# Kernel tuning notes

Measured on AMD Instinct MI355X. Metric: run time of the kernel, lower is better.

The kernel has to match this reference:

```python
import jax, jax.numpy as jnp
import numpy as np

N, D, K, P = 4096, 256, 16, 3
MAXDEG = K + 1          # self loop guarantees deg >= 1, randint caps deg <= K+1
TAU, LAM, BETA, MARGIN = 0.8, 0.5, 1.0, 0.1
EPS_PD = 1e-6           # F.pairwise_distance eps (added to the difference)


def _make_adj(k):
    nbr = jax.random.randint(k, (N, K), 0, N)
    m = jnp.zeros((N, N), jnp.float32)
    m = m.at[jnp.arange(N)[:, None], nbr].set(1.0)
    m = m.at[jnp.arange(N), jnp.arange(N)].set(1.0)
    return m / m.sum(1, keepdims=True)  # row-normalized metapath adjacency


def setup_inputs():
    key = jax.random.key(0)
    ks = jax.random.split(key, 12)
    g = 1.414 * (2.0 / (D + D)) ** 0.5  # xavier_normal gain=1.414
    return {
        "h": jax.random.normal(ks[0], (N, D), jnp.float32),
        "mps": jnp.stack([_make_adj(ks[1 + i]) for i in range(P)]),
        "W_gcn": jax.random.normal(ks[4], (P, D, D), jnp.float32) * g,
        "b_gcn": jnp.zeros((P, D), jnp.float32),
        "prelu_a": jnp.full((P,), 0.25, jnp.float32),
        "att_fc_W": jax.random.normal(ks[5], (D, D), jnp.float32) * g,
        "att_fc_b": jnp.zeros((D,), jnp.float32),
        "att_vec": jax.random.normal(ks[6], (D,), jnp.float32) * g,
        "proj_W1": jax.random.normal(ks[7], (D, D), jnp.float32) * g,
        "proj_b1": jnp.zeros((D,), jnp.float32),
        "proj_W2": jax.random.normal(ks[8], (D, D), jnp.float32) * g,
        "proj_b2": jnp.zeros((D,), jnp.float32),
    }


def _gcn(h, adj, W, b, a):
    out = adj @ (h @ W.T) + b          # spmm(adj, fc(h)) + bias
    return jnp.where(out > 0, out, a * out)  # PReLU


def _node_loss(emb, adj):
    # vectorized form of the per-node nonzero/pairwise_distance loop
    mask = adj > 0                      # [N, N]
    deg = mask.sum(1)                   # [N], >= 1 via self loops
    # stable argsort: neighbors first (ascending index), matching torch.nonzero order
    pos_idx = jnp.argsort(~mask, axis=1)[:, :MAXDEG]
    neg_idx = jnp.argsort(mask, axis=1)[:, :MAXDEG]   # first deg non-neighbors
    anc = emb[:, None, :]               # anchor expanded over pairs
    dp = jnp.sum((anc - emb[pos_idx] + EPS_PD) ** 2, -1)  # [N, MAXDEG]
    dn = jnp.sum((anc - emb[neg_idx] + EPS_PD) ** 2, -1)
    valid = jnp.arange(MAXDEG)[None, :] < deg[:, None]
    per = jnp.maximum(dp - dn + MARGIN, 0.0) * valid
    return jnp.sum(per.sum(1) / deg.astype(emb.dtype))  # per-node mean, summed


def _proj(z, W1, b1, W2, b2):
    return jax.nn.elu(z @ W1.T + b1) @ W2.T + b2


def _contrast(z1, z2, pos, W1, b1, W2, b2):
    p1 = _proj(z1, W1, b1, W2, b2)
    p2 = _proj(z2, W1, b1, W2, b2)
    n1 = jnp.linalg.norm(p1, axis=-1, keepdims=True)
    n2 = jnp.linalg.norm(p2, axis=-1, keepdims=True)
    sim = jnp.exp((p1 @ p2.T) / (n1 * n2.T) / TAU)     # [N, N]
    m12 = sim / (sim.sum(1, keepdims=True) + 1e-8)
    m21 = sim.T / (sim.T.sum(1, keepdims=True) + 1e-8)
    l12 = -jnp.log((m12 * pos).sum(-1)).mean()
    l21 = -jnp.log((m21 * pos).sum(-1)).mean()
    return LAM * l12 + (1.0 - LAM) * l21


def reference(h, mps, W_gcn, b_gcn, prelu_a, att_fc_W, att_fc_b, att_vec,
              proj_W1, proj_b1, proj_W2, proj_b2):
    embeds = [_gcn(h, mps[i], W_gcn[i], b_gcn[i], prelu_a[i]) for i in range(P)]
    node_loss = sum(_node_loss(embeds[i], mps[i]) for i in range(P))
    # faithful to original control flow: i==0 inner loop overwrites self.loss,
    # so only the (0, P-1) pair survives from i==0
    closs = _contrast(embeds[0], embeds[P - 1], mps[0], proj_W1, proj_b1, proj_W2, proj_b2)
    for i in range(1, P - 1):
        for j in range(i + 1, P):
            closs = closs + _contrast(embeds[i], embeds[j], mps[i], proj_W1, proj_b1, proj_W2, proj_b2)
    # semantic attention over metapaths
    sp = jnp.stack([jnp.tanh(e @ att_fc_W.T + att_fc_b).mean(0) for e in embeds])  # [P, D]
    beta = jax.nn.softmax(sp @ att_vec)                                            # [P]
    z_mp = jnp.einsum('p,pnd->nd', beta, jnp.stack(embeds))
    return z_mp, node_loss + BETA * closs
```

## Files before the change

kernel.cpp:

```cpp
#include <hip/hip_runtime.h>
#include <hip/hip_bf16.h>

constexpr int N = 4096;
constexpr int D = 256;
constexpr int P = 3;
constexpr int MAXDEG = 17;
constexpr float TAU = 0.8f;
constexpr float MARGIN = 0.1f;
constexpr float EPS_PD = 1e-6f;

constexpr int LDP = 40;

constexpr int OFF_H    = 0;
constexpr int OFF_WG   = 1048576;
constexpr int OFF_ATTW = 1245184;
constexpr int OFF_W1   = 1310720;
constexpr int OFF_W2   = 1376256;
constexpr int OFF_BG   = 1441792;
constexpr int OFF_ATTB = 1442560;
constexpr int OFF_AV   = 1442816;
constexpr int OFF_PA   = 1443072;
constexpr int OFF_B1   = 1443328;
constexpr int OFF_B2   = 1443584;
constexpr int CONV_TOTAL = 1443840;

typedef __attribute__((ext_vector_type(8))) short bfrag8;
typedef __attribute__((ext_vector_type(4))) float facc4;

__device__ inline facc4 mfma16(bfrag8 a, bfrag8 b, facc4 c) {
    return __builtin_amdgcn_mfma_f32_16x16x32_bf16(a, b, c, 0, 0, 0);
}
__device__ inline float b2f(__hip_bfloat16 v) { return __bfloat162float(v); }
__device__ inline float bfbits2f(unsigned short u) {
    return __uint_as_float(((unsigned int)u) << 16);
}
__device__ inline unsigned short f2bfbits(float v) {
    __hip_bfloat16 t = __float2bfloat16(v);
    return *(unsigned short*)&t;
}
__device__ inline int get_bf(const int* __restrict__ counter) { return counter[0] > 100; }

__device__ inline float load_in(const void* p, size_t i, int bf) {
    return bf ? __bfloat162float(((const __hip_bfloat16*)p)[i])
              : ((const float*)p)[i];
}

__device__ __forceinline__ void gl_lds16(const __hip_bfloat16* g, __hip_bfloat16* l) {
    __builtin_amdgcn_global_load_lds(
        (const __attribute__((address_space(1))) unsigned int*)g,
        (__attribute__((address_space(3))) unsigned int*)l, 16, 0, 0);
}

__global__ void detect_dtype(const unsigned int* __restrict__ w, int nwords,
                             int* __restrict__ counter,
                             float* __restrict__ zbuf, int nz) {
    int t0 = blockIdx.x * blockDim.x + threadIdx.x;
    if (t0 < nz) zbuf[t0] = 0.f;
    int stride = gridDim.x * blockDim.x;
    int c = 0;
    for (int i = t0; i < nwords; i += stride) {
        unsigned int x = w[i];
        if ((x & 0xFFFF0000u) == 0u && x != 0u) c++;
    }
    for (int s = 32; s > 0; s >>= 1) c += __shfl_down(c, s);
    if ((threadIdx.x & 63) == 0 && c > 0) atomicMax(counter, 1 << 20);
}

__global__ void stage2(const void* __restrict__ h, const void* __restrict__ wg,
                       const void* __restrict__ mps,
                       const void* attw, const void* w1, const void* w2,
                       const void* bg, const void* attb, const void* av,
                       const void* pa, const void* b1, const void* b2,
                       const int* __restrict__ counter,
                       __hip_bfloat16* __restrict__ conv,
                       __hip_bfloat16* __restrict__ xbuf,
                       int* __restrict__ nbr_idx, float* __restrict__ nbr_val,
                       int* __restrict__ neg_idx, int* __restrict__ deg) {
    __shared__ __align__(16) __hip_bfloat16 As[64 * LDP];
    __shared__ __align__(16) __hip_bfloat16 Bs[3][64 * LDP];
    int bid = blockIdx.x;
    int bf = get_bf(counter);
    if (bid < 256) {
        int bm = (bid & 63) * 64, bn = (bid >> 6) * 64;
        int tid = threadIdx.x, wave = tid >> 6, lane = tid & 63;
        int quad = lane >> 4, l15 = lane & 15;
        int wr = (wave & 1) * 32, wc = (wave >> 1) * 32;
        facc4 acc[3][2][2] = {};
        int sr = tid >> 2, kq = (tid & 3) * 8;
        for (int k0 = 0; k0 < D; k0 += 32) {
            if (bf) {
                *(bfrag8*)&As[sr * LDP + kq] =
                    *(const bfrag8*)((const unsigned short*)h + (size_t)(bm + sr) * D + k0 + kq);
                #pragma unroll
                for (int z = 0; z < 3; z++)
                    *(bfrag8*)&Bs[z][sr * LDP + kq] =
                        *(const bfrag8*)((const unsigned short*)wg +
                                         (size_t)z * D * D + (size_t)(bn + sr) * D + k0 + kq);
            } else {
                const float* hp = (const float*)h + (size_t)(bm + sr) * D + k0 + kq;
                float4 a0 = *(const float4*)hp, a1 = *(const float4*)(hp + 4);
                bfrag8 t;
                t[0] = f2bfbits(a0.x); t[1] = f2bfbits(a0.y);
                t[2] = f2bfbits(a0.z); t[3] = f2bfbits(a0.w);
                t[4] = f2bfbits(a1.x); t[5] = f2bfbits(a1.y);
                t[6] = f2bfbits(a1.z); t[7] = f2bfbits(a1.w);
                *(bfrag8*)&As[sr * LDP + kq] = t;
                #pragma unroll
                for (int z = 0; z < 3; z++) {
                    const float* wp = (const float*)wg +
                        (size_t)z * D * D + (size_t)(bn + sr) * D + k0 + kq;
                    float4 b0 = *(const float4*)wp, b1v = *(const float4*)(wp + 4);
                    bfrag8 u;
                    u[0] = f2bfbits(b0.x);  u[1] = f2bfbits(b0.y);
                    u[2] = f2bfbits(b0.z);  u[3] = f2bfbits(b0.w);
                    u[4] = f2bfbits(b1v.x); u[5] = f2bfbits(b1v.y);
                    u[6] = f2bfbits(b1v.z); u[7] = f2bfbits(b1v.w);
                    *(bfrag8*)&Bs[z][sr * LDP + kq] = u;
                }
            }
            __syncthreads();
            bfrag8 af[2];
            #pragma unroll
            for (int mi = 0; mi < 2; mi++)
                af[mi] = *(const bfrag8*)&As[(wr + mi * 16 + l15) * LDP + quad * 8];
            #pragma unroll
            for (int z = 0; z < 3; z++) {
                bfrag8 bfr[2];
                #pragma unroll
                for (int ni = 0; ni < 2; ni++)
                    bfr[ni] = *(const bfrag8*)&Bs[z][(wc + ni * 16 + l15) * LDP + quad * 8];
                #pragma unroll
                for (int mi = 0; mi < 2; mi++)
                    #pragma unroll
                    for (int ni = 0; ni < 2; ni++)
                        acc[z][mi][ni] = mfma16(af[mi], bfr[ni], acc[z][mi][ni]);
            }
            __syncthreads();
        }
        #pragma unroll
        for (int z = 0; z < 3; z++)
            #pragma unroll
            for (int mi = 0; mi < 2; mi++)
                #pragma unroll
                for (int ni = 0; ni < 2; ni++) {
                    int col = bn + wc + ni * 16 + l15;
                    #pragma unroll
                    for (int r = 0; r < 4; r++) {
                        int row = bm + wr + mi * 16 + quad * 4 + r;
                        xbuf[(size_t)z * N * D + (size_t)row * D + col] =
                            __float2bfloat16(acc[z][mi][ni][r]);
                    }
                }
    } else if (bid < 256 + P * N) {
        int row = bid - 256;
        int t = threadIdx.x;
        int* cnt = (int*)As;
        int* sidx = ((int*)As) + 1;
        float* sval = (float*)(((int*)As) + 33);
        if (t == 0) *cnt = 0;
        __syncthreads();
        int e0 = t * 16;
        if (bf) {
            const uint4* base = (const uint4*)((const __hip_bfloat16*)mps + (size_t)row * N + e0);
            #pragma unroll
            for (int v = 0; v < 2; v++) {
                uint4 w = base[v];
                unsigned int ws[4] = {w.x, w.y, w.z, w.w};
                #pragma unroll
                for (int j = 0; j < 4; j++) {
                    unsigned short lo = (unsigned short)(ws[j] & 0xFFFFu);
                    unsigned short hi = (unsigned short)(ws[j] >> 16);
                    if (lo) { int k = atomicAdd(cnt, 1); if (k < 32) { sidx[k] = e0 + v * 8 + j * 2;     sval[k] = bfbits2f(lo); } }
                    if (hi) { int k = atomicAdd(cnt, 1); if (k < 32) { sidx[k] = e0 + v * 8 + j * 2 + 1; sval[k] = bfbits2f(hi); } }
                }
            }
        } else {
            const float4* base = (const float4*)((const float*)mps + (size_t)row * N + e0);
            #pragma unroll
            for (int v = 0; v < 4; v++) {
                float4 w = base[v];
                float ws[4] = {w.x, w.y, w.z, w.w};
                #pragma unroll
                for (int j = 0; j < 4; j++)
                    if (ws[j] > 0.f) { int k = atomicAdd(cnt, 1); if (k < 32) { sidx[k] = e0 + v * 4 + j; sval[k] = ws[j]; } }
            }
        }
        __syncthreads();
        if (t < 64) {
            int dg = *cnt; if (dg > MAXDEG) dg = MAXDEG;
            int myidx = 0; float myval = 0.f; int rank = 0;
            if (t < dg) {
                myidx = sidx[t]; myval = sval[t];
                for (int j = 0; j < dg; j++) rank += (sidx[j] < myidx) ? 1 : 0;
            }
            if (t < dg) { sidx[rank] = myidx; sval[rank] = myval; }
            if (t < MAXDEG) {
                nbr_idx[(size_t)row * MAXDEG + t] = (t < dg) ? sidx[t] : 0;
                nbr_val[(size_t)row * MAXDEG + t] = (t < dg) ? sval[t] : 0.f;
            }
            if (t == 0) deg[row] = dg;
            int c = t;
            bool cand = (c < dg + MAXDEG);
            bool isnbr = false;
            if (cand) for (int j = 0; j < dg; j++) isnbr |= (sidx[j] == c);
            bool nonnbr = cand && !isnbr;
            unsigned long long m = __ballot(nonnbr);
            int nrank = __popcll(m & ((c < 64) ? ((1ull << c) - 1ull) : ~0ull));
            if (nonnbr && nrank < MAXDEG) neg_idx[(size_t)row * MAXDEG + nrank] = c;
        }
    } else {
        int cb = bid - (256 + P * N);
        const void* srcs[9] = {attw, w1, w2, bg, attb, av, pa, b1, b2};
        const int offs[9] = {OFF_ATTW, OFF_W1, OFF_W2, OFF_BG, OFF_ATTB,
                             OFF_AV, OFF_PA, OFF_B1, OFF_B2};
        const int lens[9] = {65536, 65536, 65536, 768, 256, 256, 3, 256, 256};
        int stride = 64 * 256;
        int t0 = cb * 256 + threadIdx.x;
        #pragma unroll
        for (int s = 0; s < 9; s++) {
            for (int i = t0; i < lens[s]; i += stride)
                conv[offs[s] + i] = __float2bfloat16(load_in(srcs[s], i, bf));
        }
    }
}

__global__ void spmm_prelu(const __hip_bfloat16* __restrict__ Xbase,
                           const int* __restrict__ nbr_idx, const float* __restrict__ nbr_val,
                           const int* __restrict__ deg, const __hip_bfloat16* __restrict__ conv,
                           __hip_bfloat16* __restrict__ embBase) {
    int z = blockIdx.z;
    int wave = threadIdx.x >> 6, lane = threadIdx.x & 63;
    int n = blockIdx.x * 4 + wave;
    const __hip_bfloat16* X = Xbase + (size_t)z * N * D;
    int dg = deg[z * N + n];
    int idxv = 0; float valv = 0.f;
    if (lane < MAXDEG) {
        idxv = nbr_idx[((size_t)z * N + n) * MAXDEG + lane];
        valv = nbr_val[((size_t)z * N + n) * MAXDEG + lane];
    }
    float acc[4] = {0.f, 0.f, 0.f, 0.f};
    int k = 0;
    for (; k + 3 < dg; k += 4) {
        int j0 = __shfl(idxv, k), j1 = __shfl(idxv, k + 1);
        int j2 = __shfl(idxv, k + 2), j3 = __shfl(idxv, k + 3);
        float v0 = __shfl(valv, k), v1 = __shfl(valv, k + 1);
        float v2 = __shfl(valv, k + 2), v3 = __shfl(valv, k + 3);
        ushort4 x0 = *(const ushort4*)&X[(size_t)j0 * D + lane * 4];
        ushort4 x1 = *(const ushort4*)&X[(size_t)j1 * D + lane * 4];
        ushort4 x2 = *(const ushort4*)&X[(size_t)j2 * D + lane * 4];
        ushort4 x3 = *(const ushort4*)&X[(size_t)j3 * D + lane * 4];
        acc[0] += v0 * bfbits2f(x0.x) + v1 * bfbits2f(x1.x) + v2 * bfbits2f(x2.x) + v3 * bfbits2f(x3.x);
        acc[1] += v0 * bfbits2f(x0.y) + v1 * bfbits2f(x1.y) + v2 * bfbits2f(x2.y) + v3 * bfbits2f(x3.y);
        acc[2] += v0 * bfbits2f(x0.z) + v1 * bfbits2f(x1.z) + v2 * bfbits2f(x2.z) + v3 * bfbits2f(x3.z);
        acc[3] += v0 * bfbits2f(x0.w) + v1 * bfbits2f(x1.w) + v2 * bfbits2f(x2.w) + v3 * bfbits2f(x3.w);
    }
    for (; k < dg; k++) {
        int j0 = __shfl(idxv, k); float v0 = __shfl(valv, k);
        ushort4 x0 = *(const ushort4*)&X[(size_t)j0 * D + lane * 4];
        acc[0] += v0 * bfbits2f(x0.x); acc[1] += v0 * bfbits2f(x0.y);
        acc[2] += v0 * bfbits2f(x0.z); acc[3] += v0 * bfbits2f(x0.w);
    }
    ushort4 bb = *(const ushort4*)&conv[OFF_BG + z * D + lane * 4];
    float a = b2f(conv[OFF_PA + z]);
    ushort4 o;
    float v0 = acc[0] + bfbits2f(bb.x); o.x = f2bfbits(v0 > 0.f ? v0 : a * v0);
    float v1 = acc[1] + bfbits2f(bb.y); o.y = f2bfbits(v1 > 0.f ? v1 : a * v1);
    float v2 = acc[2] + bfbits2f(bb.z); o.z = f2bfbits(v2 > 0.f ? v2 : a * v2);
    float v3 = acc[3] + bfbits2f(bb.w); o.w = f2bfbits(v3 > 0.f ? v3 : a * v3);
    *(ushort4*)&embBase[(size_t)z * N * D + (size_t)n * D + lane * 4] = o;
}

__global__ void gemm_dual_nl(const __hip_bfloat16* __restrict__ embBase,
                             const __hip_bfloat16* __restrict__ conv,
                             __hip_bfloat16* __restrict__ xbuf,
                             float* __restrict__ spacc,
                             const int* __restrict__ nbr_idx,
                             const int* __restrict__ neg_idx,
                             const int* __restrict__ deg,
                             float* __restrict__ nlpart) {
    __shared__ __align__(16) __hip_bfloat16 As[64 * LDP];
    __shared__ __align__(16) __hip_bfloat16 Bsa[64 * LDP];
    __shared__ __align__(16) __hip_bfloat16 Bsw[64 * LDP];
    int z = blockIdx.z;
    if (blockIdx.y < 4) {
        const __hip_bfloat16* A = embBase + (size_t)z * N * D;
        const __hip_bfloat16* Ba = conv + OFF_ATTW;
        const __hip_bfloat16* Bw = conv + OFF_W1;
        int bm = blockIdx.x * 64, bn = blockIdx.y * 64;
        int tid = threadIdx.x, wave = tid >> 6, lane = tid & 63;
        int quad = lane >> 4, l15 = lane & 15;
        int wr = (wave & 1) * 32, wc = (wave >> 1) * 32;
        facc4 accA[2][2] = {};
        facc4 accW[2][2] = {};
        int sr = tid >> 2, kq = (tid & 3) * 8;
        for (int k0 = 0; k0 < D; k0 += 32) {
            *(bfrag8*)&As[sr * LDP + kq]  = *(const bfrag8*)&A[(size_t)(bm + sr) * D + k0 + kq];
            *(bfrag8*)&Bsa[sr * LDP + kq] = *(const bfrag8*)&Ba[(size_t)(bn + sr) * D + k0 + kq];
            *(bfrag8*)&Bsw[sr * LDP + kq] = *(const bfrag8*)&Bw[(size_t)(bn + sr) * D + k0 + kq];
            __syncthreads();
            bfrag8 af[2], ba[2], bw[2];
            #pragma unroll
            for (int mi = 0; mi < 2; mi++)
                af[mi] = *(const bfrag8*)&As[(wr + mi * 16 + l15) * LDP + quad * 8];
            #pragma unroll
            for (int ni = 0; ni < 2; ni++) {
                ba[ni] = *(const bfrag8*)&Bsa[(wc + ni * 16 + l15) * LDP + quad * 8];
                bw[ni] = *(const bfrag8*)&Bsw[(wc + ni * 16 + l15) * LDP + quad * 8];
            }
            #pragma unroll
            for (int mi = 0; mi < 2; mi++)
                #pragma unroll
                for (int ni = 0; ni < 2; ni++) {
                    accA[mi][ni] = mfma16(af[mi], ba[ni], accA[mi][ni]);
                    accW[mi][ni] = mfma16(af[mi], bw[ni], accW[mi][ni]);
                }
            __syncthreads();
        }
        float cs[2] = {0.f, 0.f};
        #pragma unroll
        for (int mi = 0; mi < 2; mi++) {
            #pragma unroll
            for (int ni = 0; ni < 2; ni++) {
                int col = bn + wc + ni * 16 + l15;
                float battb = b2f(conv[OFF_ATTB + col]);
                float bb1   = b2f(conv[OFF_B1 + col]);
                #pragma unroll
                for (int r = 0; r < 4; r++) {
                    int row = bm + wr + mi * 16 + quad * 4 + r;
                    cs[ni] += tanhf(accA[mi][ni][r] + battb);
                    float v = accW[mi][ni][r] + bb1;
                    v = v > 0.f ? v : expm1f(v);
                    xbuf[(size_t)z * N * D + (size_t)row * D + col] = __float2bfloat16(v);
                }
            }
        }
        #pragma unroll
        for (int ni = 0; ni < 2; ni++) {
            float v = cs[ni];
            v += __shfl_xor(v, 16); v += __shfl_xor(v, 32);
            if (quad == 0) {
                int col = bn + wc + ni * 16 + l15;
                atomicAdd(&spacc[(size_t)z * D + col], v);
            }
        }
    } else {
        int wave = threadIdx.x >> 6, lane = threadIdx.x & 63;
        int nb = blockIdx.x * 16 + (blockIdx.y - 4);
        int n = nb * 4 + wave;
        const __hip_bfloat16* emb = embBase + (size_t)z * N * D;
        int dg = deg[z * N + n];
        int ipv = 0, igv = 0;
        if (lane < MAXDEG) {
            ipv = nbr_idx[((size_t)z * N + n) * MAXDEG + lane];
            igv = neg_idx[((size_t)z * N + n) * MAXDEG + lane];
        }
        ushort4 ar = *(const ushort4*)&emb[(size_t)n * D + lane * 4];
        float a[4] = {bfbits2f(ar.x), bfbits2f(ar.y), bfbits2f(ar.z), bfbits2f(ar.w)};
        float s = 0.f;
        int k = 0;
        for (; k + 1 < dg; k += 2) {
            int jp0 = __shfl(ipv, k), jn0 = __shfl(igv, k);
            int jp1 = __shfl(ipv, k + 1), jn1 = __shfl(igv, k + 1);
            ushort4 pr0 = *(const ushort4*)&emb[(size_t)jp0 * D + lane * 4];
            ushort4 nr0 = *(const ushort4*)&emb[(size_t)jn0 * D + lane * 4];
            ushort4 pr1 = *(const ushort4*)&emb[(size_t)jp1 * D + lane * 4];
            ushort4 nr1 = *(const ushort4*)&emb[(size_t)jn1 * D + lane * 4];
            float dp0, dn0, dp1, dn1;
            {
                float x0 = a[0] - bfbits2f(pr0.x) + EPS_PD, y0 = a[0] - bfbits2f(nr0.x) + EPS_PD;
                float x1 = a[1] - bfbits2f(pr0.y) + EPS_PD, y1 = a[1] - bfbits2f(nr0.y) + EPS_PD;
                float x2 = a[2] - bfbits2f(pr0.z) + EPS_PD, y2 = a[2] - bfbits2f(nr0.z) + EPS_PD;
                float x3 = a[3] - bfbits2f(pr0.w) + EPS_PD, y3 = a[3] - bfbits2f(nr0.w) + EPS_PD;
                dp0 = x0 * x0 + x1 * x1 + x2 * x2 + x3 * x3;
                dn0 = y0 * y0 + y1 * y1 + y2 * y2 + y3 * y3;
            }
            {
                float x0 = a[0] - bfbits2f(pr1.x) + EPS_PD, y0 = a[0] - bfbits2f(nr1.x) + EPS_PD;
                float x1 = a[1] - bfbits2f(pr1.y) + EPS_PD, y1 = a[1] - bfbits2f(nr1.y) + EPS_PD;
                float x2 = a[2] - bfbits2f(pr1.z) + EPS_PD, y2 = a[2] - bfbits2f(nr1.z) + EPS_PD;
                float x3 = a[3] - bfbits2f(pr1.w) + EPS_PD, y3 = a[3] - bfbits2f(nr1.w) + EPS_PD;
                dp1 = x0 * x0 + x1 * x1 + x2 * x2 + x3 * x3;
                dn1 = y0 * y0 + y1 * y1 + y2 * y2 + y3 * y3;
            }
            #pragma unroll
            for (int st = 1; st <= 32; st <<= 1) {
                dp0 += __shfl_xor(dp0, st); dn0 += __shfl_xor(dn0, st);
                dp1 += __shfl_xor(dp1, st); dn1 += __shfl_xor(dn1, st);
            }
            float v0 = dp0 - dn0 + MARGIN; s += v0 > 0.f ? v0 : 0.f;
            float v1 = dp1 - dn1 + MARGIN; s += v1 > 0.f ? v1 : 0.f;
        }
        if (k < dg) {
            int jp = __shfl(ipv, k), jn = __shfl(igv, k);
            ushort4 pr = *(const ushort4*)&emb[(size_t)jp * D + lane * 4];
            ushort4 nr = *(const ushort4*)&emb[(size_t)jn * D + lane * 4];
            float x0 = a[0] - bfbits2f(pr.x) + EPS_PD, y0 = a[0] - bfbits2f(nr.x) + EPS_PD;
            float x1 = a[1] - bfbits2f(pr.y) + EPS_PD, y1 = a[1] - bfbits2f(nr.y) + EPS_PD;
            float x2 = a[2] - bfbits2f(pr.z) + EPS_PD, y2 = a[2] - bfbits2f(nr.z) + EPS_PD;
            float x3 = a[3] - bfbits2f(pr.w) + EPS_PD, y3 = a[3] - bfbits2f(nr.w) + EPS_PD;
            float dp = x0 * x0 + x1 * x1 + x2 * x2 + x3 * x3;
            float dn = y0 * y0 + y1 * y1 + y2 * y2 + y3 * y3;
            #pragma unroll
            for (int st = 1; st <= 32; st <<= 1) { dp += __shfl_xor(dp, st); dn += __shfl_xor(dn, st); }
            float v = dp - dn + MARGIN;
            s += v > 0.f ? v : 0.f;
        }
        if (lane == 0) nlpart[z * N + n] = s / (float)dg;
    }
}

__global__ void gemm_w2_norm(const __hip_bfloat16* __restrict__ xbase,
                             const __hip_bfloat16* __restrict__ conv,
                             __hip_bfloat16* __restrict__ qbase) {
    int z = blockIdx.z;
    const __hip_bfloat16* A = xbase + (size_t)z * N * D;
    const __hip_bfloat16* B = conv + OFF_W2;
    __shared__ __align__(16) __hip_bfloat16 As[16 * LDP];
    __shared__ __align__(16) __hip_bfloat16 Bs[256 * LDP];
    __shared__ float sred[4][16];
    int bm = blockIdx.x * 16;
    int tid = threadIdx.x, wave = tid >> 6, lane = tid & 63;
    int quad = lane >> 4, l15 = lane & 15;
    int wc = wave * 64;
    facc4 acc[4] = {};
    for (int k0 = 0; k0 < D; k0 += 32) {
        if (tid < 64) {
            int r = tid >> 2, kq = (tid & 3) * 8;
            *(bfrag8*)&As[r * LDP + kq] = *(const bfrag8*)&A[(size_t)(bm + r) * D + k0 + kq];
        }
        #pragma unroll
        for (int i = 0; i < 4; i++) {
            int f = tid + 256 * i;
            int r = f >> 2, kq = (f & 3) * 8;
            *(bfrag8*)&Bs[r * LDP + kq] = *(const bfrag8*)&B[(size_t)r * D + k0 + kq];
        }
        __syncthreads();
        bfrag8 af = *(const bfrag8*)&As[l15 * LDP + quad * 8];
        #pragma unroll
        for (int ni = 0; ni < 4; ni++) {
            bfrag8 bf = *(const bfrag8*)&Bs[(wc + ni * 16 + l15) * LDP + quad * 8];
            acc[ni] = mfma16(af, bf, acc[ni]);
        }
        __syncthreads();
    }
    float vv[4][4];
    #pragma unroll
    for (int ni = 0; ni < 4; ni++) {
        float bb = b2f(conv[OFF_B2 + wc + ni * 16 + l15]);
        #pragma unroll
        for (int r = 0; r < 4; r++) vv[ni][r] = acc[ni][r] + bb;
    }
    #pragma unroll
    for (int r = 0; r < 4; r++) {
        float ss = vv[0][r] * vv[0][r] + vv[1][r] * vv[1][r] +
                   vv[2][r] * vv[2][r] + vv[3][r] * vv[3][r];
        ss += __shfl_xor(ss, 1); ss += __shfl_xor(ss, 2);
        ss += __shfl_xor(ss, 4); ss += __shfl_xor(ss, 8);
        if (l15 == 0) sred[wave][quad * 4 + r] = ss;
    }
    __syncthreads();
    #pragma unroll
    for (int r = 0; r < 4; r++) {
        int rl = quad * 4 + r;
        float ssum = sred[0][rl] + sred[1][rl] + sred[2][rl] + sred[3][rl];
        float inv = rsqrtf(ssum + 1e-30f);
        int row = bm + rl;
        #pragma unroll
        for (int ni = 0; ni < 4; ni++)
            qbase[(size_t)z * N * D + (size_t)row * D + wc + ni * 16 + l15] =
                __float2bfloat16(vv[ni][r] * inv);
    }
}

__global__ void sim_pd_zmp(const __hip_bfloat16* __restrict__ q,
                           float* __restrict__ rowsum, float* __restrict__ colsum,
                           const __hip_bfloat16* __restrict__ embBase,
                           const int* __restrict__ nbr_idx, const float* __restrict__ nbr_val,
                           const int* __restrict__ deg,
                           float* __restrict__ pdrow, float* __restrict__ pdcol,
                           const float* __restrict__ spacc,
                           const __hip_bfloat16* __restrict__ conv,
                           const int* __restrict__ counter,
                           void* __restrict__ out) {
    __shared__ __align__(16) __hip_bfloat16 As[128 * 64];
    __shared__ __align__(16) __hip_bfloat16 Bs[128 * 64];
    int pair = blockIdx.z;
    int y = blockIdx.y;
    if (y < 32) {
        const __hip_bfloat16* Qa = q + (size_t)pair * N * D;
        const __hip_bfloat16* Qb = q + (size_t)2 * N * D;
        int bm = blockIdx.x * 128, bn = y * 128;
        int tid = threadIdx.x, wave = tid >> 6, lane = tid & 63;
        int quad = lane >> 4, l15 = lane & 15;
        int wr = (wave & 1) * 64, wc = (wave >> 1) * 64;
        facc4 acc[4][4] = {};
        int sr0 = tid >> 3;
        int cc  = tid & 7;
        for (int k0 = 0; k0 < D; k0 += 64) {
            #pragma unroll
            for (int i = 0; i < 4; i++) {
                int r = sr0 + 32 * i;
                int cg = (cc ^ (r & 7)) * 8;
                gl_lds16(&Qa[(size_t)(bm + r) * D + k0 + cg], &As[r * 64 + cc * 8]);
                gl_lds16(&Qb[(size_t)(bn + r) * D + k0 + cg], &Bs[r * 64 + cc * 8]);
            }
            __syncthreads();
            #pragma unroll
            for (int kk = 0; kk < 64; kk += 32) {
                int kb = kk >> 3;
                bfrag8 af[4], bfr[4];
                #pragma unroll
                for (int mi = 0; mi < 4; mi++) {
                    int R = wr + mi * 16 + l15;
                    int pc = ((kb + quad) ^ (l15 & 7)) * 8;
                    af[mi] = *(const bfrag8*)&As[R * 64 + pc];
                }
                #pragma unroll
                for (int ni = 0; ni < 4; ni++) {
                    int R = wc + ni * 16 + l15;
                    int pc = ((kb + quad) ^ (l15 & 7)) * 8;
                    bfr[ni] = *(const bfrag8*)&Bs[R * 64 + pc];
                }
                #pragma unroll
                for (int mi = 0; mi < 4; mi++)
                    #pragma unroll
                    for (int ni = 0; ni < 4; ni++)
                        acc[mi][ni] = mfma16(af[mi], bfr[ni], acc[mi][ni]);
            }
            __syncthreads();
        }
        constexpr float invtau = 1.0f / TAU;
        float rs[4][4];
        float cs[4] = {0.f, 0.f, 0.f, 0.f};
        #pragma unroll
        for (int mi = 0; mi < 4; mi++)
            #pragma unroll
            for (int r = 0; r < 4; r++) rs[mi][r] = 0.f;
        #pragma unroll
        for (int mi = 0; mi < 4; mi++)
            #pragma unroll
            for (int ni = 0; ni < 4; ni++)
                #pragma unroll
                for (int r = 0; r < 4; r++) {
                    float e = __expf(acc[mi][ni][r] * invtau);
                    rs[mi][r] += e;
                    cs[ni] += e;
                }
        #pragma unroll
        for (int mi = 0; mi < 4; mi++)
            #pragma unroll
            for (int r = 0; r < 4; r++) {
                float v = rs[mi][r];
                v += __shfl_xor(v, 1); v += __shfl_xor(v, 2);
                v += __shfl_xor(v, 4); v += __shfl_xor(v, 8);
                rs[mi][r] = v;
            }
        if (l15 == 0) {
            #pragma unroll
            for (int mi = 0; mi < 4; mi++)
                #pragma unroll
                for (int r = 0; r < 4; r++)
                    atomicAdd(&rowsum[(size_t)pair * N + bm + wr + mi * 16 + quad * 4 + r], rs[mi][r]);
        }
        #pragma unroll
        for (int ni = 0; ni < 4; ni++) {
            float v = cs[ni];
            v += __shfl_xor(v, 16); v += __shfl_xor(v, 32);
            if (quad == 0)
                atomicAdd(&colsum[(size_t)pair * N + bn + wc + ni * 16 + l15], v);
        }
    } else if (y < 64) {
        int wave = threadIdx.x >> 6, lane = threadIdx.x & 63;
        int nb = blockIdx.x * 32 + (y - 32);
        int n = nb * 4 + wave;
        const __hip_bfloat16* Qa = q + (size_t)pair * N * D;
        const __hip_bfloat16* Qb = q + (size_t)2 * N * D;
        int dg = deg[pair * N + n];
        int idxv = 0; float valv = 0.f;
        if (lane < MAXDEG) {
            idxv = nbr_idx[((size_t)pair * N + n) * MAXDEG + lane];
            valv = nbr_val[((size_t)pair * N + n) * MAXDEG + lane];
        }
        const float invtau = 1.0f / TAU;
        ushort4 ar = *(const ushort4*)&Qa[(size_t)n * D + lane * 4];
        ushort4 br = *(const ushort4*)&Qb[(size_t)n * D + lane * 4];
        float a[4] = {bfbits2f(ar.x), bfbits2f(ar.y), bfbits2f(ar.z), bfbits2f(ar.w)};
        float b[4] = {bfbits2f(br.x), bfbits2f(br.y), bfbits2f(br.z), bfbits2f(br.w)};
        float sr = 0.f, sc = 0.f;
        int k = 0;
        for (; k + 1 < dg; k += 2) {
            int j0 = __shfl(idxv, k), j1 = __shfl(idxv, k + 1);
            float vk0 = __shfl(valv, k), vk1 = __shfl(valv, k + 1);
            ushort4 pj0 = *(const ushort4*)&Qb[(size_t)j0 * D + lane * 4];
            ushort4 aj0 = *(const ushort4*)&Qa[(size_t)j0 * D + lane * 4];
            ushort4 pj1 = *(const ushort4*)&Qb[(size_t)j1 * D + lane * 4];
            ushort4 aj1 = *(const ushort4*)&Qa[(size_t)j1 * D + lane * 4];
            float dr0 = a[0] * bfbits2f(pj0.x) + a[1] * bfbits2f(pj0.y) +
                        a[2] * bfbits2f(pj0.z) + a[3] * bfbits2f(pj0.w);
            float dc0 = b[0] * bfbits2f(aj0.x) + b[1] * bfbits2f(aj0.y) +
                        b[2] * bfbits2f(aj0.z) + b[3] * bfbits2f(aj0.w);
            float dr1 = a[0] * bfbits2f(pj1.x) + a[1] * bfbits2f(pj1.y) +
                        a[2] * bfbits2f(pj1.z) + a[3] * bfbits2f(pj1.w);
            float dc1 = b[0] * bfbits2f(aj1.x) + b[1] * bfbits2f(aj1.y) +
                        b[2] * bfbits2f(aj1.z) + b[3] * bfbits2f(aj1.w);
            #pragma unroll
            for (int s2 = 1; s2 <= 32; s2 <<= 1) {
                dr0 += __shfl_xor(dr0, s2); dc0 += __shfl_xor(dc0, s2);
                dr1 += __shfl_xor(dr1, s2); dc1 += __shfl_xor(dc1, s2);
            }
            sr += __expf(dr0 * invtau) * vk0 + __expf(dr1 * invtau) * vk1;
            sc += __expf(dc0 * invtau) * vk0 + __expf(dc1 * invtau) * vk1;
        }
        if (k < dg) {
            int j = __shfl(idxv, k);
            float vk = __shfl(valv, k);
            ushort4 pj = *(const ushort4*)&Qb[(size_t)j * D + lane * 4];
            ushort4 aj = *(const ushort4*)&Qa[(size_t)j * D + lane * 4];
            float dr = a[0] * bfbits2f(pj.x) + a[1] * bfbits2f(pj.y) +
                       a[2] * bfbits2f(pj.z) + a[3] * bfbits2f(pj.w);
            float dc = b[0] * bfbits2f(aj.x) + b[1] * bfbits2f(aj.y) +
                       b[2] * bfbits2f(aj.z) + b[3] * bfbits2f(aj.w);
            #pragma unroll
            for (int s2 = 1; s2 <= 32; s2 <<= 1) { dr += __shfl_xor(dr, s2); dc += __shfl_xor(dc, s2); }
            sr += __expf(dr * invtau) * vk;
            sc += __expf(dc * invtau) * vk;
        }
        if (lane == 0) { pdrow[pair * N + n] = sr; pdcol[pair * N + n] = sc; }
    } else {
        int bf = get_bf(counter);
        int t = threadIdx.x;
        float* red = (float*)As;
        float* w   = (float*)Bs;
        for (int p = 0; p < P; p++) {
            float v = (spacc[p * D + t] / (float)N) * b2f(conv[OFF_AV + t]);
            red[t] = v;
            __syncthreads();
            for (int s = 128; s > 0; s >>= 1) { if (t < s) red[t] += red[t + s]; __syncthreads(); }
            if (t == 0) w[p] = red[0];
            __syncthreads();
        }
        float m = fmaxf(w[0], fmaxf(w[1], w[2]));
        float e0 = __expf(w[0] - m), e1 = __expf(w[1] - m), e2 = __expf(w[2] - m);
        float ssum = e0 + e1 + e2;
        float b0 = e0 / ssum, b1 = e1 / ssum, b2 = e2 / ssum;
        int slice = pair * 32 + blockIdx.x;
        int base = slice * (N * D / 64);
        for (int e = t * 4; e < N * D / 64; e += 256 * 4) {
            int i = base + e;
            ushort4 x0 = *(const ushort4*)&embBase[i];
            ushort4 x1 = *(const ushort4*)&embBase[(size_t)N * D + i];
            ushort4 x2 = *(const ushort4*)&embBase[(size_t)2 * N * D + i];
            float v[4];
            v[0] = b0 * bfbits2f(x0.x) + b1 * bfbits2f(x1.x) + b2 * bfbits2f(x2.x);
            v[1] = b0 * bfbits2f(x0.y) + b1 * bfbits2f(x1.y) + b2 * bfbits2f(x2.y);
            v[2] = b0 * bfbits2f(x0.z) + b1 * bfbits2f(x1.z) + b2 * bfbits2f(x2.z);
            v[3] = b0 * bfbits2f(x0.w) + b1 * bfbits2f(x1.w) + b2 * bfbits2f(x2.w);
            if (bf) {
                ushort4 ov;
                ov.x = f2bfbits(v[0]); ov.y = f2bfbits(v[1]);
                ov.z = f2bfbits(v[2]); ov.w = f2bfbits(v[3]);
                *(ushort4*)&((__hip_bfloat16*)out)[i] = ov;
            } else {
                float* o = (float*)out;
                o[i] = v[0]; o[i + 1] = v[1]; o[i + 2] = v[2]; o[i + 3] = v[3];
            }
        }
    }
}

__global__ void finalize_loss(const float* __restrict__ nlpart,
                              const float* __restrict__ rowsum, const float* __restrict__ colsum,
                              const float* __restrict__ pdrow, const float* __restrict__ pdcol,
                              const int* __restrict__ counter,
                              void* __restrict__ out) {
    int bf = get_bf(counter);
    int t = threadIdx.x;
    __shared__ float red[256];
    float s = 0.f;
    for (int i = t; i < P * N; i += 256) s += nlpart[i];
    for (int i = t; i < 2 * N; i += 256) {
        float l12 = -logf(pdrow[i] / (rowsum[i] + 1e-8f));
        float l21 = -logf(pdcol[i] / (colsum[i] + 1e-8f));
        s += (0.5f * l12 + 0.5f * l21) / (float)N;
    }
    red[t] = s;
    __syncthreads();
    for (int st = 128; st > 0; st >>= 1) { if (t < st) red[t] += red[t + st]; __syncthreads(); }
    if (t == 0) {
        if (bf) ((__hip_bfloat16*)out)[(size_t)N * D] = __float2bfloat16(red[0]);
        else    ((float*)out)[(size_t)N * D] = red[0];
    }
}

extern "C" void kernel_launch(void* const* d_in, const int* in_sizes, int n_in,
                              void* d_out, int out_size, void* d_ws, size_t ws_size,
                              hipStream_t stream) {
    const void* h        = d_in[0];
    const void* mps      = d_in[1];
    const void* W_gcn    = d_in[2];
    const void* b_gcn    = d_in[3];
    const void* prelu_a  = d_in[4];
    const void* att_fc_W = d_in[5];
    const void* att_fc_b = d_in[6];
    const void* att_vec  = d_in[7];
    const void* proj_W1  = d_in[8];
    const void* proj_b1  = d_in[9];
    const void* proj_W2  = d_in[10];
    const void* proj_b2  = d_in[11];

    char* ws = (char*)d_ws;
    size_t off = 0;
    auto alloc = [&](size_t bytes) -> char* {
        char* p = ws + off;
        off = (off + bytes + 255) & ~(size_t)255;
        return p;
    };
    __hip_bfloat16* conv = (__hip_bfloat16*)alloc((size_t)CONV_TOTAL * 2);
    __hip_bfloat16* xbuf = (__hip_bfloat16*)alloc((size_t)P * N * D * 2);
    __hip_bfloat16* emb  = (__hip_bfloat16*)alloc((size_t)P * N * D * 2);
    __hip_bfloat16* q    = (__hip_bfloat16*)alloc((size_t)P * N * D * 2);
    int*   nbr_idx = (int*)alloc((size_t)P * N * MAXDEG * 4);
    float* nbr_val = (float*)alloc((size_t)P * N * MAXDEG * 4);
    int*   neg_idx = (int*)alloc((size_t)P * N * MAXDEG * 4);
    int*   deg     = (int*)alloc((size_t)P * N * 4);
    float* nlpart  = (float*)alloc((size_t)P * N * 4);
    float* pdrow   = (float*)alloc((size_t)2 * N * 4);
    float* pdcol   = (float*)alloc((size_t)2 * N * 4);
    char* zero_begin = ws + off;
    float* rowsum = (float*)alloc((size_t)2 * N * 4);
    float* colsum = (float*)alloc((size_t)2 * N * 4);
    float* spacc  = (float*)alloc((size_t)P * D * 4);
    size_t zero_bytes = (size_t)((ws + off) - zero_begin);
    int*   counter = (int*)alloc(16);

    detect_dtype<<<1024, 256, 0, stream>>>((const unsigned int*)mps, 2 * 1024 * 1024,
                                           counter, (float*)zero_begin,
                                           (int)(zero_bytes / 4));

    stage2<<<256 + P * N + 64, 256, 0, stream>>>(h, W_gcn, mps,
                                                 att_fc_W, proj_W1, proj_W2, b_gcn,
                                                 att_fc_b, att_vec, prelu_a, proj_b1, proj_b2,
                                                 counter, conv, xbuf,
                                                 nbr_idx, nbr_val, neg_idx, deg);

    spmm_prelu<<<dim3(N / 4, 1, P), 256, 0, stream>>>(xbuf, nbr_idx, nbr_val, deg, conv, emb);

    gemm_dual_nl<<<dim3(64, 20, P), 256, 0, stream>>>(emb, conv, xbuf, spacc,
                                                      nbr_idx, neg_idx, deg, nlpart);

    gemm_w2_norm<<<dim3(N / 16, 1, P), 256, 0, stream>>>(xbuf, conv, q);

    sim_pd_zmp<<<dim3(32, 65, 2), 256, 0, stream>>>(q, rowsum, colsum, emb,
                                                    nbr_idx, nbr_val, deg,
                                                    pdrow, pdcol, spacc, conv,
                                                    counter, d_out);

    finalize_loss<<<1, 256, 0, stream>>>(nlpart, rowsum, colsum, pdrow, pdcol,
                                         counter, d_out);
}
```

Baseline: 458.5 us.

## Share Qb tile across both contrast pairs and batch four neighbors per wave

The similarity GEMM in sim_pd_zmp now computes both pairs (q0·q2 and q1·q2) in one block, loading the shared Qb tile once into LDS and reusing its B fragments for two accumulator sets. The grid changes from a z=2 launch to a single flattened y dimension. The node-loss and positive-diagonal gather loops switch from one neighbor per wave with 4 elements per lane to four neighbors per wave, using 16 lanes each with 16-element uint4 loads, which shortens the shuffle reductions and issues more loads in parallel. The cost is higher register pressure from two 4x4 accumulator arrays and 16-float anchor arrays, plus extra LDS, which may lower occupancy.

```diff
diff --git a/kernel.cpp b/kernel.cpp
--- a/kernel.cpp
+++ b/kernel.cpp
@@ -11,8 +11,6 @@
 
 constexpr int LDP = 40;
 
-constexpr int OFF_H    = 0;
-constexpr int OFF_WG   = 1048576;
 constexpr int OFF_ATTW = 1245184;
 constexpr int OFF_W1   = 1310720;
 constexpr int OFF_W2   = 1376256;
@@ -43,6 +41,13 @@
 __device__ inline float load_in(const void* p, size_t i, int bf) {
     return bf ? __bfloat162float(((const __hip_bfloat16*)p)[i])
               : ((const float*)p)[i];
+}
+
+__device__ inline void unpack8(uint4 w, float* f) {
+    f[0] = bfbits2f((unsigned short)(w.x & 0xFFFFu)); f[1] = bfbits2f((unsigned short)(w.x >> 16));
+    f[2] = bfbits2f((unsigned short)(w.y & 0xFFFFu)); f[3] = bfbits2f((unsigned short)(w.y >> 16));
+    f[4] = bfbits2f((unsigned short)(w.z & 0xFFFFu)); f[5] = bfbits2f((unsigned short)(w.z >> 16));
+    f[6] = bfbits2f((unsigned short)(w.w & 0xFFFFu)); f[7] = bfbits2f((unsigned short)(w.w >> 16));
 }
 
 __device__ __forceinline__ void gl_lds16(const __hip_bfloat16* g, __hip_bfloat16* l) {
@@ -345,6 +350,7 @@
         }
     } else {
         int wave = threadIdx.x >> 6, lane = threadIdx.x & 63;
+        int g = lane >> 4, u = lane & 15;
         int nb = blockIdx.x * 16 + (blockIdx.y - 4);
         int n = nb * 4 + wave;
         const __hip_bfloat16* emb = embBase + (size_t)z * N * D;
@@ -354,57 +360,42 @@
             ipv = nbr_idx[((size_t)z * N + n) * MAXDEG + lane];
             igv = neg_idx[((size_t)z * N + n) * MAXDEG + lane];
         }
-        ushort4 ar = *(const ushort4*)&emb[(size_t)n * D + lane * 4];
-        float a[4] = {bfbits2f(ar.x), bfbits2f(ar.y), bfbits2f(ar.z), bfbits2f(ar.w)};
+        float a[16];
+        {
+            const uint4* ap = (const uint4*)&emb[(size_t)n * D + u * 16];
+            unpack8(ap[0], a); unpack8(ap[1], a + 8);
+        }
         float s = 0.f;
-        int k = 0;
-        for (; k + 1 < dg; k += 2) {
-            int jp0 = __shfl(ipv, k), jn0 = __shfl(igv, k);
-            int jp1 = __shfl(ipv, k + 1), jn1 = __shfl(igv, k + 1);
-            ushort4 pr0 = *(const ushort4*)&emb[(size_t)jp0 * D + lane * 4];
-            ushort4 nr0 = *(const ushort4*)&emb[(size_t)jn0 * D + lane * 4];
-            ushort4 pr1 = *(const ushort4*)&emb[(size_t)jp1 * D + lane * 4];
-            ushort4 nr1 = *(const ushort4*)&emb[(size_t)jn1 * D + lane * 4];
-            float dp0, dn0, dp1, dn1;
-            {
-                float x0 = a[0] - bfbits2f(pr0.x) + EPS_PD, y0 = a[0] - bfbits2f(nr0.x) + EPS_PD;
-                float x1 = a[1] - bfbits2f(pr0.y) + EPS_PD, y1 = a[1] - bfbits2f(nr0.y) + EPS_PD;
-                float x2 = a[2] - bfbits2f(pr0.z) + EPS_PD, y2 = a[2] - bfbits2f(nr0.z) + EPS_PD;
-                float x3 = a[3] - bfbits2f(pr0.w) + EPS_PD, y3 = a[3] - bfbits2f(nr0.w) + EPS_PD;
-                dp0 = x0 * x0 + x1 * x1 + x2 * x2 + x3 * x3;
-                dn0 = y0 * y0 + y1 * y1 + y2 * y2 + y3 * y3;
-            }
-            {
-                float x0 = a[0] - bfbits2f(pr1.x) + EPS_PD, y0 = a[0] - bfbits2f(nr1.x) + EPS_PD;
-                float x1 = a[1] - bfbits2f(pr1.y) + EPS_PD, y1 = a[1] - bfbits2f(nr1.y) + EPS_PD;
-                float x2 = a[2] - bfbits2f(pr1.z) + EPS_PD, y2 = a[2] - bfbits2f(nr1.z) + EPS_PD;
-                float x3 = a[3] - bfbits2f(pr1.w) + EPS_PD, y3 = a[3] - bfbits2f(nr1.w) + EPS_PD;
-                dp1 = x0 * x0 + x1 * x1 + x2 * x2 + x3 * x3;
-                dn1 = y0 * y0 + y1 * y1 + y2 * y2 + y3 * y3;
-            }
-            #pragma unroll
-            for (int st = 1; st <= 32; st <<= 1) {
-                dp0 += __shfl_xor(dp0, st); dn0 += __shfl_xor(dn0, st);
-                dp1 += __shfl_xor(dp1, st); dn1 += __shfl_xor(dn1, st);
-            }
-            float v0 = dp0 - dn0 + MARGIN; s += v0 > 0.f ? v0 : 0.f;
-            float v1 = dp1 - dn1 + MARGIN; s += v1 > 0.f ? v1 : 0.f;
-        }
-        if (k < dg) {
-            int jp = __shfl(ipv, k), jn = __shfl(igv, k);
-            ushort4 pr = *(const ushort4*)&emb[(size_t)jp * D + lane * 4];
-            ushort4 nr = *(const ushort4*)&emb[(size_t)jn * D + lane * 4];
-            float x0 = a[0] - bfbits2f(pr.x) + EPS_PD, y0 = a[0] - bfbits2f(nr.x) + EPS_PD;
-            float x1 = a[1] - bfbits2f(pr.y) + EPS_PD, y1 = a[1] - bfbits2f(nr.y) + EPS_PD;
-            float x2 = a[2] - bfbits2f(pr.z) + EPS_PD, y2 = a[2] - bfbits2f(nr.z) + EPS_PD;
-            float x3 = a[3] - bfbits2f(pr.w) + EPS_PD, y3 = a[3] - bfbits2f(nr.w) + EPS_PD;
-            float dp = x0 * x0 + x1 * x1 + x2 * x2 + x3 * x3;
-            float dn = y0 * y0 + y1 * y1 + y2 * y2 + y3 * y3;
-            #pragma unroll
-            for (int st = 1; st <= 32; st <<= 1) { dp += __shfl_xor(dp, st); dn += __shfl_xor(dn, st); }
+        for (int k0 = 0; k0 < dg; k0 += 4) {
+            int k = k0 + g;
+            bool act = k < dg;
+            int kc = k < MAXDEG ? k : MAXDEG - 1;
+            int jp = __shfl(ipv, kc), jn = __shfl(igv, kc);
+            const uint4* pp = (const uint4*)&emb[(size_t)jp * D + u * 16];
+            const uint4* np = (const uint4*)&emb[(size_t)jn * D + u * 16];
+            uint4 p0 = pp[0], p1 = pp[1], q0 = np[0], q1 = np[1];
+            float pf[8], nf[8];
+            float dp = 0.f, dn = 0.f;
+            unpack8(p0, pf); unpack8(q0, nf);
+            #pragma unroll
+            for (int d = 0; d < 8; d++) {
+                float x = a[d] - pf[d] + EPS_PD; dp += x * x;
+                float y = a[d] - nf[d] + EPS_PD; dn += y * y;
+            }
+            unpack8(p1, pf); unpack8(q1, nf);
+            #pragma unroll
+            for (int d = 0; d < 8; d++) {
+                float x = a[d + 8] - pf[d] + EPS_PD; dp += x * x;
+                float y = a[d + 8] - nf[d] + EPS_PD; dn += y * y;
+            }
+            dp += __shfl_xor(dp, 1); dn += __shfl_xor(dn, 1);
+            dp += __shfl_xor(dp, 2); dn += __shfl_xor(dn, 2);
+            dp += __shfl_xor(dp, 4); dn += __shfl_xor(dn, 4);
+            dp += __shfl_xor(dp, 8); dn += __shfl_xor(dn, 8);
             float v = dp - dn + MARGIN;
-            s += v > 0.f ? v : 0.f;
-        }
+            s += (act && v > 0.f) ? v : 0.f;
+        }
+        s += __shfl_xor(s, 16); s += __shfl_xor(s, 32);
         if (lane == 0) nlpart[z * N + n] = s / (float)dg;
     }
 }
@@ -482,18 +473,21 @@
                            const __hip_bfloat16* __restrict__ conv,
                            const int* __restrict__ counter,
                            void* __restrict__ out) {
-    __shared__ __align__(16) __hip_bfloat16 As[128 * 64];
+    __shared__ __align__(16) __hip_bfloat16 As0[128 * 64];
+    __shared__ __align__(16) __hip_bfloat16 As1[128 * 64];
     __shared__ __align__(16) __hip_bfloat16 Bs[128 * 64];
-    int pair = blockIdx.z;
     int y = blockIdx.y;
+    constexpr float invtau = 1.0f / TAU;
     if (y < 32) {
-        const __hip_bfloat16* Qa = q + (size_t)pair * N * D;
+        const __hip_bfloat16* Q0 = q;
+        const __hip_bfloat16* Q1 = q + (size_t)N * D;
         const __hip_bfloat16* Qb = q + (size_t)2 * N * D;
         int bm = blockIdx.x * 128, bn = y * 128;
         int tid = threadIdx.x, wave = tid >> 6, lane = tid & 63;
         int quad = lane >> 4, l15 = lane & 15;
         int wr = (wave & 1) * 64, wc = (wave >> 1) * 64;
-        facc4 acc[4][4] = {};
+        facc4 acc0[4][4] = {};
+        facc4 acc1[4][4] = {};
         int sr0 = tid >> 3;
         int cc  = tid & 7;
         for (int k0 = 0; k0 < D; k0 += 64) {
@@ -501,77 +495,139 @@
             for (int i = 0; i < 4; i++) {
                 int r = sr0 + 32 * i;
                 int cg = (cc ^ (r & 7)) * 8;
-                gl_lds16(&Qa[(size_t)(bm + r) * D + k0 + cg], &As[r * 64 + cc * 8]);
+                gl_lds16(&Q0[(size_t)(bm + r) * D + k0 + cg], &As0[r * 64 + cc * 8]);
+                gl_lds16(&Q1[(size_t)(bm + r) * D + k0 + cg], &As1[r * 64 + cc * 8]);
                 gl_lds16(&Qb[(size_t)(bn + r) * D + k0 + cg], &Bs[r * 64 + cc * 8]);
             }
             __syncthreads();
             #pragma unroll
             for (int kk = 0; kk < 64; kk += 32) {
                 int kb = kk >> 3;
-                bfrag8 af[4], bfr[4];
-                #pragma unroll
-                for (int mi = 0; mi < 4; mi++) {
-                    int R = wr + mi * 16 + l15;
-                    int pc = ((kb + quad) ^ (l15 & 7)) * 8;
-                    af[mi] = *(const bfrag8*)&As[R * 64 + pc];
-                }
+                bfrag8 bfr[4];
                 #pragma unroll
                 for (int ni = 0; ni < 4; ni++) {
                     int R = wc + ni * 16 + l15;
                     int pc = ((kb + quad) ^ (l15 & 7)) * 8;
                     bfr[ni] = *(const bfrag8*)&Bs[R * 64 + pc];
                 }
+                {
+                    bfrag8 af[4];
+                    #pragma unroll
+                    for (int mi = 0; mi < 4; mi++) {
+                        int R = wr + mi * 16 + l15;
+                        int pc = ((kb + quad) ^ (l15 & 7)) * 8;
+                        af[mi] = *(const bfrag8*)&As0[R * 64 + pc];
+                    }
+                    #pragma unroll
+                    for (int mi = 0; mi < 4; mi++)
+                        #pragma unroll
+                        for (int ni = 0; ni < 4; ni++)
+                            acc0[mi][ni] = mfma16(af[mi], bfr[ni], acc0[mi][ni]);
+                }
+                {
+                    bfrag8 af[4];
+                    #pragma unroll
+                    for (int mi = 0; mi < 4; mi++) {
+                        int R = wr + mi * 16 + l15;
+                        int pc = ((kb + quad) ^ (l15 & 7)) * 8;
+                        af[mi] = *(const bfrag8*)&As1[R * 64 + pc];
+                    }
+                    #pragma unroll
+                    for (int mi = 0; mi < 4; mi++)
+                        #pragma unroll
+                        for (int ni = 0; ni < 4; ni++)
+                            acc1[mi][ni] = mfma16(af[mi], bfr[ni], acc1[mi][ni]);
+                }
+            }
+            __syncthreads();
+        }
+        {
+            float rs[4][4];
+            float cs[4] = {0.f, 0.f, 0.f, 0.f};
+            #pragma unroll
+            for (int mi = 0; mi < 4; mi++)
+                #pragma unroll
+                for (int r = 0; r < 4; r++) rs[mi][r] = 0.f;
+            #pragma unroll
+            for (int mi = 0; mi < 4; mi++)
+                #pragma unroll
+                for (int ni = 0; ni < 4; ni++)
+                    #pragma unroll
+                    for (int r = 0; r < 4; r++) {
+                        float e = __expf(acc0[mi][ni][r] * invtau);
+                        rs[mi][r] += e;
+                        cs[ni] += e;
+                    }
+            #pragma unroll
+            for (int mi = 0; mi < 4; mi++)
+                #pragma unroll
+                for (int r = 0; r < 4; r++) {
+                    float v = rs[mi][r];
+                    v += __shfl_xor(v, 1); v += __shfl_xor(v, 2);
+                    v += __shfl_xor(v, 4); v += __shfl_xor(v, 8);
+                    rs[mi][r] = v;
+                }
+            if (l15 == 0) {
                 #pragma unroll
                 for (int mi = 0; mi < 4; mi++)
                     #pragma unroll
-                    for (int ni = 0; ni < 4; ni++)
-                        acc[mi][ni] = mfma16(af[mi], bfr[ni], acc[mi][ni]);
-            }
-            __syncthreads();
-        }
-        constexpr float invtau = 1.0f / TAU;
-        float rs[4][4];
-        float cs[4] = {0.f, 0.f, 0.f, 0.f};
-        #pragma unroll
-        for (int mi = 0; mi < 4; mi++)
-            #pragma unroll
-            for (int r = 0; r < 4; r++) rs[mi][r] = 0.f;
-        #pragma unroll
-        for (int mi = 0; mi < 4; mi++)
-            #pragma unroll
-            for (int ni = 0; ni < 4; ni++)
+                    for (int r = 0; r < 4; r++)
+                        atomicAdd(&rowsum[bm + wr + mi * 16 + quad * 4 + r], rs[mi][r]);
+            }
+            #pragma unroll
+            for (int ni = 0; ni < 4; ni++) {
+                float v = cs[ni];
+                v += __shfl_xor(v, 16); v += __shfl_xor(v, 32);
+                if (quad == 0)
+                    atomicAdd(&colsum[bn + wc + ni * 16 + l15], v);
+            }
+        }
+        {
+            float rs[4][4];
+            float cs[4] = {0.f, 0.f, 0.f, 0.f};
+            #pragma unroll
+            for (int mi = 0; mi < 4; mi++)
+                #pragma unroll
+                for (int r = 0; r < 4; r++) rs[mi][r] = 0.f;
+            #pragma unroll
+            for (int mi = 0; mi < 4; mi++)
+                #pragma unroll
+                for (int ni = 0; ni < 4; ni++)
+                    #pragma unroll
+                    for (int r = 0; r < 4; r++) {
+                        float e = __expf(acc1[mi][ni][r] * invtau);
+                        rs[mi][r] += e;
+                        cs[ni] += e;
+                    }
+            #pragma unroll
+            for (int mi = 0; mi < 4; mi++)
                 #pragma unroll
                 for (int r = 0; r < 4; r++) {
-                    float e = __expf(acc[mi][ni][r] * invtau);
-                    rs[mi][r] += e;
-                    cs[ni] += e;
-                }
-        #pragma unroll
-        for (int mi = 0; mi < 4; mi++)
-            #pragma unroll
-            for (int r = 0; r < 4; r++) {
-                float v = rs[mi][r];
-                v += __shfl_xor(v, 1); v += __shfl_xor(v, 2);
-                v += __shfl_xor(v, 4); v += __shfl_xor(v, 8);
-                rs[mi][r] = v;
-            }
-        if (l15 == 0) {
-            #pragma unroll
-            for (int mi = 0; mi < 4; mi++)
-                #pragma unroll
-                for (int r = 0; r < 4; r++)
-                    atomicAdd(&rowsum[(size_t)pair * N + bm + wr + mi * 16 + quad * 4 + r], rs[mi][r]);
-        }
-        #pragma unroll
-        for (int ni = 0; ni < 4; ni++) {
-            float v = cs[ni];
-            v += __shfl_xor(v, 16); v += __shfl_xor(v, 32);
-            if (quad == 0)
-                atomicAdd(&colsum[(size_t)pair * N + bn + wc + ni * 16 + l15], v);
-        }
-    } else if (y < 64) {
+                    float v = rs[mi][r];
+                    v += __shfl_xor(v, 1); v += __shfl_xor(v, 2);
+                    v += __shfl_xor(v, 4); v += __shfl_xor(v, 8);
+                    rs[mi][r] = v;
+                }
+            if (l15 == 0) {
+                #pragma unroll
+                for (int mi = 0; mi < 4; mi++)
+                    #pragma unroll
+                    for (int r = 0; r < 4; r++)
+                        atomicAdd(&rowsum[N + bm + wr + mi * 16 + quad * 4 + r], rs[mi][r]);
+            }
+            #pragma unroll
+            for (int ni = 0; ni < 4; ni++) {
+                float v = cs[ni];
+                v += __shfl_xor(v, 16); v += __shfl_xor(v, 32);
+                if (quad == 0)
+                    atomicAdd(&colsum[N + bn + wc + ni * 16 + l15], v);
+            }
+        }
+    } else if (y < 96) {
+        int pair = (y - 32) >> 5;
         int wave = threadIdx.x >> 6, lane = threadIdx.x & 63;
-        int nb = blockIdx.x * 32 + (y - 32);
+        int g = lane >> 4, u = lane & 15;
+        int nb = ((y - 32) & 31) * 32 + blockIdx.x;
         int n = nb * 4 + wave;
         const __hip_bfloat16* Qa = q + (size_t)pair * N * D;
         const __hip_bfloat16* Qb = q + (size_t)2 * N * D;
@@ -581,56 +637,48 @@
             idxv = nbr_idx[((size_t)pair * N + n) * MAXDEG + lane];
             valv = nbr_val[((size_t)pair * N + n) * MAXDEG + lane];
         }
-        const float invtau = 1.0f / TAU;
-        ushort4 ar = *(const ushort4*)&Qa[(size_t)n * D + lane * 4];
-        ushort4 br = *(const ushort4*)&Qb[(size_t)n * D + lane * 4];
-        float a[4] = {bfbits2f(ar.x), bfbits2f(ar.y), bfbits2f(ar.z), bfbits2f(ar.w)};
-        float b[4] = {bfbits2f(br.x), bfbits2f(br.y), bfbits2f(br.z), bfbits2f(br.w)};
+        float a[16], b[16];
+        {
+            const uint4* ap = (const uint4*)&Qa[(size_t)n * D + u * 16];
+            unpack8(ap[0], a); unpack8(ap[1], a + 8);
+            const uint4* bp = (const uint4*)&Qb[(size_t)n * D + u * 16];
+            unpack8(bp[0], b); unpack8(bp[1], b + 8);
+        }
         float sr = 0.f, sc = 0.f;
-        int k = 0;
-        for (; k + 1 < dg; k += 2) {
-            int j0 = __shfl(idxv, k), j1 = __shfl(idxv, k + 1);
-            float vk0 = __shfl(valv, k), vk1 = __shfl(valv, k + 1);
-            ushort4 pj0 = *(const ushort4*)&Qb[(size_t)j0 * D + lane * 4];
-            ushort4 aj0 = *(const ushort4*)&Qa[(size_t)j0 * D + lane * 4];
-            ushort4 pj1 = *(const ushort4*)&Qb[(size_t)j1 * D + lane * 4];
-            ushort4 aj1 = *(const ushort4*)&Qa[(size_t)j1 * D + lane * 4];
-            float dr0 = a[0] * bfbits2f(pj0.x) + a[1] * bfbits2f(pj0.y) +
-                        a[2] * bfbits2f(pj0.z) + a[3] * bfbits2f(pj0.w);
-            float dc0 = b[0] * bfbits2f(aj0.x) + b[1] * bfbits2f(aj0.y) +
-                        b[2] * bfbits2f(aj0.z) + b[3] * bfbits2f(aj0.w);
-            float dr1 = a[0] * bfbits2f(pj1.x) + a[1] * bfbits2f(pj1.y) +
-                        a[2] * bfbits2f(pj1.z) + a[3] * bfbits2f(pj1.w);
-            float dc1 = b[0] * bfbits2f(aj1.x) + b[1] * bfbits2f(aj1.y) +
-                        b[2] * bfbits2f(aj1.z) + b[3] * bfbits2f(aj1.w);
-            #pragma unroll
-            for (int s2 = 1; s2 <= 32; s2 <<= 1) {
-                dr0 += __shfl_xor(dr0, s2); dc0 += __shfl_xor(dc0, s2);
-                dr1 += __shfl_xor(dr1, s2); dc1 += __shfl_xor(dc1, s2);
-            }
-            sr += __expf(dr0 * invtau) * vk0 + __expf(dr1 * invtau) * vk1;
-            sc += __expf(dc0 * invtau) * vk0 + __expf(dc1 * invtau) * vk1;
-        }
-        if (k < dg) {
-            int j = __shfl(idxv, k);
-            float vk = __shfl(valv, k);
-            ushort4 pj = *(const ushort4*)&Qb[(size_t)j * D + lane * 4];
-            ushort4 aj = *(const ushort4*)&Qa[(size_t)j * D + lane * 4];
-            float dr = a[0] * bfbits2f(pj.x) + a[1] * bfbits2f(pj.y) +
-                       a[2] * bfbits2f(pj.z) + a[3] * bfbits2f(pj.w);
-            float dc = b[0] * bfbits2f(aj.x) + b[1] * bfbits2f(aj.y) +
-                       b[2] * bfbits2f(aj.z) + b[3] * bfbits2f(aj.w);
-            #pragma unroll
-            for (int s2 = 1; s2 <= 32; s2 <<= 1) { dr += __shfl_xor(dr, s2); dc += __shfl_xor(dc, s2); }
-            sr += __expf(dr * invtau) * vk;
-            sc += __expf(dc * invtau) * vk;
-        }
+        for (int k0 = 0; k0 < dg; k0 += 4) {
+            int k = k0 + g;
+            bool act = k < dg;
+            int kc = k < MAXDEG ? k : MAXDEG - 1;
+            int j = __shfl(idxv, kc);
+            float vk = __shfl(valv, kc);
+            const uint4* pj = (const uint4*)&Qb[(size_t)j * D + u * 16];
+            const uint4* aj = (const uint4*)&Qa[(size_t)j * D + u * 16];
+            uint4 p0 = pj[0], p1 = pj[1], r0 = aj[0], r1 = aj[1];
+            float pf[8], af_[8];
+            float dr = 0.f, dc = 0.f;
+            unpack8(p0, pf); unpack8(r0, af_);
+            #pragma unroll
+            for (int d = 0; d < 8; d++) { dr += a[d] * pf[d]; dc += b[d] * af_[d]; }
+            unpack8(p1, pf); unpack8(r1, af_);
+            #pragma unroll
+            for (int d = 0; d < 8; d++) { dr += a[d + 8] * pf[d]; dc += b[d + 8] * af_[d]; }
+            dr += __shfl_xor(dr, 1); dc += __shfl_xor(dc, 1);
+            dr += __shfl_xor(dr, 2); dc += __shfl_xor(dc, 2);
+            dr += __shfl_xor(dr, 4); dc += __shfl_xor(dc, 4);
+            dr += __shfl_xor(dr, 8); dc += __shfl_xor(dc, 8);
+            if (act) {
+                sr += __expf(dr * invtau) * vk;
+                sc += __expf(dc * invtau) * vk;
+            }
+        }
+        sr += __shfl_xor(sr, 16); sr += __shfl_xor(sr, 32);
+        sc += __shfl_xor(sc, 16); sc += __shfl_xor(sc, 32);
         if (lane == 0) { pdrow[pair * N + n] = sr; pdcol[pair * N + n] = sc; }
     } else {
         int bf = get_bf(counter);
         int t = threadIdx.x;
-        float* red = (float*)As;
-        float* w   = (float*)Bs;
+        float* red = (float*)As0;
+        float* w   = (float*)As1;
         for (int p = 0; p < P; p++) {
             float v = (spacc[p * D + t] / (float)N) * b2f(conv[OFF_AV + t]);
             red[t] = v;
@@ -643,7 +691,7 @@
         float e0 = __expf(w[0] - m), e1 = __expf(w[1] - m), e2 = __expf(w[2] - m);
         float ssum = e0 + e1 + e2;
         float b0 = e0 / ssum, b1 = e1 / ssum, b2 = e2 / ssum;
-        int slice = pair * 32 + blockIdx.x;
+        int slice = (y - 96) * 32 + blockIdx.x;
         int base = slice * (N * D / 64);
         for (int e = t * 4; e < N * D / 64; e += 256 * 4) {
             int i = base + e;
@@ -750,7 +798,7 @@
 
     gemm_w2_norm<<<dim3(N / 16, 1, P), 256, 0, stream>>>(xbuf, conv, q);
 
-    sim_pd_zmp<<<dim3(32, 65, 2), 256, 0, stream>>>(q, rowsum, colsum, emb,
+    sim_pd_zmp<<<dim3(32, 98, 1), 256, 0, stream>>>(q, rowsum, colsum, emb,
                                                     nbr_idx, nbr_val, deg,
                                                     pdrow, pdcol, spacc, conv,
                                                     counter, d_out);
```

Measured after the change: 525.7 us. 14.7% more time.
